# Optimization experiments

Hardware: AMD Instinct MI355X
Metric: run time of the kernel (lower is better)

Reference implementation:

```python
import jax, jax.numpy as jnp
import numpy as np
import math

N_HEAD = 12
BLOCK = 256  # local attention block size (ls)
EPS = 1e-6


def _rotate(x):
    # pairs (a, b) -> (-b, a) over last dim (matches rotate_embeddings)
    a = x[..., 0::2]
    b = x[..., 1::2]
    return jnp.stack([-b, a], axis=-1).reshape(x.shape)


def setup_inputs() -> dict:
    key = jax.random.key(0)
    k1, k2, k3 = jax.random.split(key, 3)
    B, T, C = 4, 8192, 768
    s = 0.02
    return {
        "x": jax.random.normal(k1, (B, T, C), jnp.float32),
        "w_qkv": jax.random.normal(k2, (C, 3 * C), jnp.float32) * s,
        "w_ln": jnp.ones((C,), jnp.float32),
        "w_proj": jax.random.normal(k3, (C, C), jnp.float32) * s,
    }


def reference(x, w_qkv, w_ln, w_proj):
    B, T, C = x.shape
    nh, ls = N_HEAD, BLOCK
    hd = C // nh
    ng = T // ls

    xb = x.reshape(B, ng, ls, C)
    qkv = xb @ w_qkv                                   # (B,ng,ls,3C)
    q, k, v = jnp.split(qkv, 3, axis=-1)

    # QK RMSNorm over full embedding dim (before head split)
    def rms(t):
        return t * jax.lax.rsqrt(jnp.mean(t * t, axis=-1, keepdims=True) + EPS) * w_ln
    q, k = rms(q), rms(k)

    # split heads: (B,ng,nh,ls,hd)
    def heads(t):
        return jnp.swapaxes(t.reshape(B, ng, ls, nh, hd), 2, 3)
    q, k, v = heads(q), heads(k), heads(v)

    # RoPE (repo layout: freqs tiled via cat((ts,ts)), interleaved pair rotation)
    pos = 10000.0 ** ((-2.0 * jnp.arange(0, hd, 2, dtype=jnp.float32) - 1.0) / hd)
    ts = jnp.arange(ls, dtype=jnp.float32)[:, None] * pos[None, :]   # (ls, hd/2)
    rot = jnp.concatenate([ts, ts], axis=-1)                          # (ls, hd)
    cos, sin = jnp.cos(rot), jnp.sin(rot)
    q = q * cos + _rotate(q) * sin
    k = k * cos + _rotate(k) * sin

    # block-causal scores: causal only within each local block
    scale = 1.0 / math.sqrt(hd)
    att = jnp.einsum('bgnqd,bgnkd->bgnqk', q, k) * scale              # (B,ng,nh,ls,ls)
    mask = jnp.tril(jnp.ones((ls, ls), dtype=bool))
    att = jnp.where(mask, att, -jnp.finfo(att.dtype).max)
    att = jax.nn.softmax(att, axis=-1)
    y = jnp.einsum('bgnqk,bgnkd->bgnqd', att, v)                      # (B,ng,nh,ls,hd)

    y = jnp.swapaxes(y, 2, 3).reshape(B, ng, ls, C)
    y = y @ w_proj
    return y.reshape(B, T, C)
```

## Files before the change

kernel.cpp:

```cpp
#include <hip/hip_runtime.h>
#include <math.h>

typedef __attribute__((ext_vector_type(8))) short bf16x8;
typedef __attribute__((ext_vector_type(4))) short bf16x4;
typedef __attribute__((ext_vector_type(2))) short bf16x2;
typedef __attribute__((ext_vector_type(4))) float f32x4;

#define NH 12
#define HD 64
#define C0 768
#define C3 2304
#define LS 256

static __device__ __forceinline__ float bf2f(short u) {
  union { unsigned int i; float f; } c;
  c.i = ((unsigned int)(unsigned short)u) << 16;
  return c.f;
}
static __device__ __forceinline__ short f2bf(float f) {
  union { float f; unsigned int i; } c; c.f = f;
  unsigned int x = c.i;
  x += 0x7fffu + ((x >> 16) & 1u);
  return (short)(x >> 16);
}
static __device__ __forceinline__ unsigned pk2(float a, float b) {
  return (unsigned)(unsigned short)f2bf(a) | ((unsigned)(unsigned short)f2bf(b) << 16);
}

static __device__ __forceinline__ void gload_lds16(const short* g, const short* l) {
  unsigned long long ga = (unsigned long long)g;
  unsigned int la = (unsigned int)(unsigned long long)l;
  __builtin_amdgcn_global_load_lds(
      (const __attribute__((address_space(1))) void*)ga,
      (__attribute__((address_space(3))) void*)la, 16, 0, 0);
}

__global__ __launch_bounds__(256) void cast_kernel(const float* __restrict__ in,
                                                   short* __restrict__ out, int nquads) {
  int i = blockIdx.x * blockDim.x + threadIdx.x;
  int stride = gridDim.x * blockDim.x;
  for (; i < nquads; i += stride) {
    float4 v = ((const float4*)in)[i];
    bf16x4 o = { f2bf(v.x), f2bf(v.y), f2bf(v.z), f2bf(v.w) };
    ((bf16x4*)out)[i] = o;
  }
}

__global__ __launch_bounds__(256) void cast_transpose_kernel(const float* __restrict__ in,
                                                             short* __restrict__ out,
                                                             int K, int N) {
  __shared__ float tile[32][33];
  int n0 = blockIdx.x * 32, k0 = blockIdx.y * 32;
  int tx = threadIdx.x & 31, ty = threadIdx.x >> 5;
#pragma unroll
  for (int i = 0; i < 32; i += 8)
    tile[ty + i][tx] = in[(long)(k0 + ty + i) * N + n0 + tx];
  __syncthreads();
#pragma unroll
  for (int i = 0; i < 32; i += 8)
    out[(long)(n0 + ty + i) * K + k0 + tx] = f2bf(tile[tx][ty + i]);
}

__global__ void rope_tab_kernel(float* __restrict__ cost, float* __restrict__ sint) {
  int t = blockIdx.x, d = threadIdx.x;
  int i = d & 31;
  float freq = powf(10000.0f, -(float)(4 * i + 1) / 64.0f);
  float th = (float)t * freq;
  cost[t * 64 + d] = cosf(th);
  sint[t * 64 + d] = sinf(th);
}

template <int OUT_F32>
__global__ __launch_bounds__(256) void gemm_kernel(const short* __restrict__ A,
                                                   const short* __restrict__ Bt,
                                                   void* __restrict__ Cout,
                                                   int N, int K) {
  __shared__ short As[128 * 64];
  __shared__ short Bs[128 * 64];
  int bn = blockIdx.x, bm = blockIdx.y;
  int t = threadIdx.x, lane = t & 63, wave = t >> 6;
  int lr = lane & 15, lg = lane >> 4;
  int wm = (wave >> 1) * 64, wn = (wave & 1) * 64;
  const short* Abase = A + (long)bm * 128 * K;
  const short* Bbase = Bt + (long)bn * 128 * K;

  f32x4 zero4 = {0.f, 0.f, 0.f, 0.f};
  f32x4 acc[4][4];
#pragma unroll
  for (int m = 0; m < 4; ++m)
#pragma unroll
    for (int n = 0; n < 4; ++n) acc[m][n] = zero4;

  int srow[4], scol[4];
#pragma unroll
  for (int i = 0; i < 4; ++i) {
    int q = i * 256 + t;
    int r = q >> 3, cp = q & 7;
    srow[i] = r;
    scol[i] = (cp ^ (r & 7)) * 8;
  }

  for (int kt = 0; kt < K / 64; ++kt) {
    int k0 = kt * 64;
#pragma unroll
    for (int i = 0; i < 4; ++i) {
      int q = i * 256 + t;
      gload_lds16(Abase + (long)srow[i] * K + k0 + scol[i], &As[q * 8]);
      gload_lds16(Bbase + (long)srow[i] * K + k0 + scol[i], &Bs[q * 8]);
    }
    asm volatile("s_waitcnt vmcnt(0)" ::: "memory");
    __syncthreads();

#pragma unroll
    for (int s = 0; s < 2; ++s) {
      bf16x8 af[4], bfv[4];
#pragma unroll
      for (int m = 0; m < 4; ++m) {
        int row = wm + m * 16 + lr;
        af[m] = *(bf16x8*)&As[row * 64 + (((s * 4 + lg) ^ (row & 7)) << 3)];
      }
#pragma unroll
      for (int n = 0; n < 4; ++n) {
        int row = wn + n * 16 + lr;
        bfv[n] = *(bf16x8*)&Bs[row * 64 + (((s * 4 + lg) ^ (row & 7)) << 3)];
      }
#pragma unroll
      for (int m = 0; m < 4; ++m)
#pragma unroll
        for (int n = 0; n < 4; ++n)
          acc[m][n] = __builtin_amdgcn_mfma_f32_16x16x32_bf16(af[m], bfv[n], acc[m][n], 0, 0, 0);
    }
    __syncthreads();
  }

  long crow0 = (long)bm * 128 + wm;
  long ccol0 = (long)bn * 128 + wn;
#pragma unroll
  for (int m = 0; m < 4; ++m)
#pragma unroll
    for (int n = 0; n < 4; ++n)
#pragma unroll
      for (int r = 0; r < 4; ++r) {
        long row = crow0 + m * 16 + lg * 4 + r;
        long col = ccol0 + n * 16 + lr;
        float v = acc[m][n][r];
        if (OUT_F32) ((float*)Cout)[row * N + col] = v;
        else ((short*)Cout)[row * N + col] = f2bf(v);
      }
}

__global__ __launch_bounds__(384) void norm_rope_kernel(short* __restrict__ QKV,
    const float* __restrict__ w_ln, const float* __restrict__ cost,
    const float* __restrict__ sint) {
  int row = blockIdx.x;
  int t = row & 255;
  int i = threadIdx.x;
  long base = (long)row * C3;
  bf16x2 q2 = *(bf16x2*)&QKV[base + 2 * i];
  bf16x2 k2 = *(bf16x2*)&QKV[base + C0 + 2 * i];
  float qa = bf2f(q2.x), qb = bf2f(q2.y);
  float ka = bf2f(k2.x), kb = bf2f(k2.y);
  float sq = qa * qa + qb * qb;
  float sk = ka * ka + kb * kb;
#pragma unroll
  for (int o = 32; o > 0; o >>= 1) {
    sq += __shfl_down(sq, o);
    sk += __shfl_down(sk, o);
  }
  __shared__ float red[2][6];
  int wv = i >> 6;
  if ((i & 63) == 0) { red[0][wv] = sq; red[1][wv] = sk; }
  __syncthreads();
  float s0 = 0.f, s1 = 0.f;
#pragma unroll
  for (int w = 0; w < 6; ++w) { s0 += red[0][w]; s1 += red[1][w]; }
  float rq = rsqrtf(s0 * (1.0f / 768.0f) + 1e-6f);
  float rk = rsqrtf(s1 * (1.0f / 768.0f) + 1e-6f);
  float wl0 = w_ln[2 * i], wl1 = w_ln[2 * i + 1];
  float qn0 = qa * rq * wl0, qn1 = qb * rq * wl1;
  float kn0 = ka * rk * wl0, kn1 = kb * rk * wl1;
  int d0 = (2 * i) & 63;
  float c0 = cost[t * 64 + d0], c1 = cost[t * 64 + d0 + 1];
  float s0r = sint[t * 64 + d0], s1r = sint[t * 64 + d0 + 1];
  bf16x2 qo, ko;
  qo.x = f2bf(qn0 * c0 - qn1 * s0r);
  qo.y = f2bf(qn1 * c1 + qn0 * s1r);
  ko.x = f2bf(kn0 * c0 - kn1 * s0r);
  ko.y = f2bf(kn1 * c1 + kn0 * s1r);
  *(bf16x2*)&QKV[base + 2 * i] = qo;
  *(bf16x2*)&QKV[base + C0 + 2 * i] = ko;
}

__global__ __launch_bounds__(512, 3) void attn_kernel(const short* __restrict__ QKV,
                                                      short* __restrict__ Y) {
  __shared__ short Ks[256 * 64];
  __shared__ short Vt[64 * 256];
  int blk = blockIdx.x;
  int bg = blk / NH, h = blk % NH;
  const long base = (long)bg * LS * C3 + h * HD;
  int tid = threadIdx.x, lane = tid & 63, wave = tid >> 6;
  int lr = lane & 15, lg = lane >> 4;

#pragma unroll
  for (int it = 0; it < 4; ++it) {
    int q = it * 512 + tid;
    int row = q >> 3, cp = q & 7;
    int gcp = cp ^ (row & 7);
    gload_lds16(QKV + base + (long)row * C3 + C0 + gcp * 8, &Ks[q * 8]);
  }
#pragma unroll
  for (int it = 0; it < 8; ++it) {
    int e = tid * 4 + it * 2048;
    int k = e >> 6, n = e & 63;
    bf16x4 v = *(const bf16x4*)&QKV[base + (long)k * C3 + 2 * C0 + n];
#pragma unroll
    for (int j = 0; j < 4; ++j) {
      int nn = n + j;
      Vt[nn * 256 + (((k >> 3) ^ (nn & 7)) << 3) + (k & 7)] = v[j];
    }
  }
  asm volatile("s_waitcnt vmcnt(0)" ::: "memory");
  __syncthreads();

  int addrA = (((lane >> 4) & 1) * 32 + lr) * 4;
  int addrB = addrA + 64;
  bool selhi = (lane & 32) != 0;

  for (int tt = 0; tt < 2; ++tt) {
    int tile = (tt == 0) ? wave : (15 - wave);
    int m0 = tile * 16;
    bf16x8 qf[2];
#pragma unroll
    for (int ks = 0; ks < 2; ++ks)
      qf[ks] = *(const bf16x8*)&QKV[base + (long)(m0 + lr) * C3 + ks * 32 + lg * 8];

    f32x4 zero4 = {0.f, 0.f, 0.f, 0.f};
    f32x4 accs[16];
#pragma unroll
    for (int n = 0; n < 16; ++n) accs[n] = zero4;

    __builtin_amdgcn_s_setprio(1);
#pragma unroll
    for (int n = 0; n < 16; ++n) {
      if (n <= tile) {
        int row = n * 16 + lr, sw = row & 7;
        bf16x8 k0 = *(bf16x8*)&Ks[row * 64 + ((lg ^ sw) << 3)];
        bf16x8 k1 = *(bf16x8*)&Ks[row * 64 + (((4 + lg) ^ sw) << 3)];
        accs[n] = __builtin_amdgcn_mfma_f32_16x16x32_bf16(k0, qf[0], accs[n], 0, 0, 0);
        accs[n] = __builtin_amdgcn_mfma_f32_16x16x32_bf16(k1, qf[1], accs[n], 0, 0, 0);
      }
    }
    __builtin_amdgcn_s_setprio(0);

    float mloc = -1e30f;
#pragma unroll
    for (int n = 0; n < 16; ++n) {
      if (n <= tile) {
#pragma unroll
        for (int r = 0; r < 4; ++r) {
          float v = accs[n][r];
          if (n == tile) v = (lg * 4 + r <= lr) ? v : -1e30f;
          accs[n][r] = v;
          mloc = fmaxf(mloc, v);
        }
      }
    }
    mloc = fmaxf(mloc, __shfl_xor(mloc, 16));
    mloc = fmaxf(mloc, __shfl_xor(mloc, 32));
    float s = 0.f;
#pragma unroll
    for (int n = 0; n < 16; ++n) {
      if (n <= tile) {
#pragma unroll
        for (int r = 0; r < 4; ++r) {
          float p = __expf((accs[n][r] - mloc) * 0.125f);
          accs[n][r] = p;
          s += p;
        }
      }
    }
    s += __shfl_xor(s, 16);
    s += __shfl_xor(s, 32);
    float rs = 1.0f / s;
    float rv[4];
#pragma unroll
    for (int r = 0; r < 4; ++r) {
      union { float f; int i; } c; c.f = rs;
      union { int i; float f; } o;
      o.i = __builtin_amdgcn_ds_bpermute((lg * 4 + r) * 4, c.i);
      rv[r] = o.f;
    }

    int ktmax = (m0 + 15) >> 5;
    f32x4 yacc[4];
#pragma unroll
    for (int n2 = 0; n2 < 4; ++n2) yacc[n2] = zero4;
#pragma unroll
    for (int kt = 0; kt < 8; ++kt) {
      if (kt <= ktmax) {
        int n0 = 2 * kt, n1 = 2 * kt + 1;
        unsigned a01_0 = pk2(accs[n0][0], accs[n0][1]);
        unsigned a23_0 = pk2(accs[n0][2], accs[n0][3]);
        unsigned a01_1 = (n1 <= tile) ? pk2(accs[n1][0], accs[n1][1]) : 0u;
        unsigned a23_1 = (n1 <= tile) ? pk2(accs[n1][2], accs[n1][3]) : 0u;
        union { unsigned u[4]; bf16x8 v; } af;
        unsigned g0a = (unsigned)__builtin_amdgcn_ds_bpermute(addrA, (int)a01_0);
        unsigned g0b = (unsigned)__builtin_amdgcn_ds_bpermute(addrA, (int)a01_1);
        unsigned g1a = (unsigned)__builtin_amdgcn_ds_bpermute(addrA, (int)a23_0);
        unsigned g1b = (unsigned)__builtin_amdgcn_ds_bpermute(addrA, (int)a23_1);
        unsigned g2a = (unsigned)__builtin_amdgcn_ds_bpermute(addrB, (int)a01_0);
        unsigned g2b = (unsigned)__builtin_amdgcn_ds_bpermute(addrB, (int)a01_1);
        unsigned g3a = (unsigned)__builtin_amdgcn_ds_bpermute(addrB, (int)a23_0);
        unsigned g3b = (unsigned)__builtin_amdgcn_ds_bpermute(addrB, (int)a23_1);
        af.u[0] = selhi ? g0b : g0a;
        af.u[1] = selhi ? g1b : g1a;
        af.u[2] = selhi ? g2b : g2a;
        af.u[3] = selhi ? g3b : g3a;
        int ac = kt * 32 + lg * 8;
        __builtin_amdgcn_s_setprio(1);
#pragma unroll
        for (int n2 = 0; n2 < 4; ++n2) {
          int vn = n2 * 16 + lr;
          bf16x8 vb = *(bf16x8*)&Vt[vn * 256 + (((ac >> 3) ^ (vn & 7)) << 3)];
          yacc[n2] = __builtin_amdgcn_mfma_f32_16x16x32_bf16(af.v, vb, yacc[n2], 0, 0, 0);
        }
        __builtin_amdgcn_s_setprio(0);
      }
    }

#pragma unroll
    for (int n2 = 0; n2 < 4; ++n2) {
#pragma unroll
      for (int r = 0; r < 4; ++r) {
        int row = m0 + lg * 4 + r, d = n2 * 16 + lr;
        Y[((long)(bg * LS + row)) * C0 + h * HD + d] = f2bf(yacc[n2][r] * rv[r]);
      }
    }
  }
}

extern "C" void kernel_launch(void* const* d_in, const int* in_sizes, int n_in,
                              void* d_out, int out_size, void* d_ws, size_t ws_size,
                              hipStream_t stream) {
  (void)in_sizes; (void)n_in; (void)out_size; (void)ws_size;
  const float* x = (const float*)d_in[0];
  const float* w_qkv = (const float*)d_in[1];
  const float* w_ln = (const float*)d_in[2];
  const float* w_proj = (const float*)d_in[3];
  float* out = (float*)d_out;

  char* ws = (char*)d_ws;
  short* Xb      = (short*)(ws + 0);
  short* QKV     = (short*)(ws + 50331648);
  short* Yb      = (short*)(ws + 201326592);
  short* WqkvT   = (short*)(ws + 251658240);
  short* WprojT  = (short*)(ws + 255197184);
  float* cost    = (float*)(ws + 256376832);
  float* sint    = (float*)(ws + 256442368);

  cast_kernel<<<2048, 256, 0, stream>>>(x, Xb, (4 * 8192 * C0) / 4);
  cast_transpose_kernel<<<dim3(C3 / 32, C0 / 32), 256, 0, stream>>>(w_qkv, WqkvT, C0, C3);
  cast_transpose_kernel<<<dim3(C0 / 32, C0 / 32), 256, 0, stream>>>(w_proj, WprojT, C0, C0);
  rope_tab_kernel<<<256, 64, 0, stream>>>(cost, sint);

  gemm_kernel<0><<<dim3(C3 / 128, 32768 / 128), 256, 0, stream>>>(Xb, WqkvT, QKV, C3, C0);
  norm_rope_kernel<<<32768, 384, 0, stream>>>(QKV, w_ln, cost, sint);
  attn_kernel<<<128 * NH, 512, 0, stream>>>(QKV, Yb);
  gemm_kernel<1><<<dim3(C0 / 128, 32768 / 128), 256, 0, stream>>>(Yb, WprojT, out, C0, C0);
}
```

Before: 352.6 us.

## Replace GEMM with 256x256-tile, 8-wave, double-buffered pipelined MFMA kernel

Replaces the 128x128 single-buffered GEMM with a 256x256 tile kernel using 8 waves, a double-buffered 128KB LDS, fine-grained staged global-to-LDS loads interleaved with MFMA phases, s_setprio scheduling, and an XCD-aware block remapping. It is meant to hide global load latency and improve data reuse for both the QKV and output projections. Risks include the large LDS footprint limiting occupancy, and correctness depends on the vmcnt bookkeeping. For the 768-wide projection, only 384 blocks are launched.

```diff
diff --git a/kernel.cpp b/kernel.cpp
--- a/kernel.cpp
+++ b/kernel.cpp
@@ -70,80 +70,123 @@
   sint[t * 64 + d] = sinf(th);
 }
 
+#define PH_PRE                                         \
+  __builtin_amdgcn_s_barrier();                        \
+  asm volatile("s_waitcnt lgkmcnt(0)" ::: "memory");   \
+  __builtin_amdgcn_sched_barrier(0);                   \
+  __builtin_amdgcn_s_setprio(1);
+#define PH_POST                                        \
+  __builtin_amdgcn_s_setprio(0);                       \
+  __builtin_amdgcn_s_barrier();
+#define PH_POSTV                                       \
+  __builtin_amdgcn_s_setprio(0);                       \
+  asm volatile("s_waitcnt vmcnt(4)" ::: "memory");     \
+  __builtin_amdgcn_s_barrier();
+#define MMQ(MH, NP, AF)                                                            \
+  { _Pragma("unroll") for (int f_ = 0; f_ < 4; ++f_)                               \
+      _Pragma("unroll") for (int n_ = 0; n_ < 2; ++n_)                             \
+        _Pragma("unroll") for (int k_ = 0; k_ < 2; ++k_)                           \
+          acc[(MH)*4 + f_][(NP)*2 + n_] = __builtin_amdgcn_mfma_f32_16x16x32_bf16( \
+              AF[f_*2 + k_], bfv[((NP)*2 + n_)*2 + k_],                            \
+              acc[(MH)*4 + f_][(NP)*2 + n_], 0, 0, 0); }
+
 template <int OUT_F32>
-__global__ __launch_bounds__(256) void gemm_kernel(const short* __restrict__ A,
-                                                   const short* __restrict__ Bt,
-                                                   void* __restrict__ Cout,
-                                                   int N, int K) {
-  __shared__ short As[128 * 64];
-  __shared__ short Bs[128 * 64];
-  int bn = blockIdx.x, bm = blockIdx.y;
+__global__ __launch_bounds__(512, 2) void gemm8p_kernel(const short* __restrict__ A,
+                                                        const short* __restrict__ Bt,
+                                                        void* __restrict__ Cout,
+                                                        int N, int K, int nbn) {
+  __shared__ short lds[65536];
   int t = threadIdx.x, lane = t & 63, wave = t >> 6;
   int lr = lane & 15, lg = lane >> 4;
-  int wm = (wave >> 1) * 64, wn = (wave & 1) * 64;
-  const short* Abase = A + (long)bm * 128 * K;
-  const short* Bbase = Bt + (long)bn * 128 * K;
-
-  f32x4 zero4 = {0.f, 0.f, 0.f, 0.f};
-  f32x4 acc[4][4];
-#pragma unroll
-  for (int m = 0; m < 4; ++m)
-#pragma unroll
-    for (int n = 0; n < 4; ++n) acc[m][n] = zero4;
-
-  int srow[4], scol[4];
-#pragma unroll
-  for (int i = 0; i < 4; ++i) {
-    int q = i * 256 + t;
-    int r = q >> 3, cp = q & 7;
-    srow[i] = r;
-    scol[i] = (cp ^ (r & 7)) * 8;
-  }
-
-  for (int kt = 0; kt < K / 64; ++kt) {
-    int k0 = kt * 64;
-#pragma unroll
-    for (int i = 0; i < 4; ++i) {
-      int q = i * 256 + t;
-      gload_lds16(Abase + (long)srow[i] * K + k0 + scol[i], &As[q * 8]);
-      gload_lds16(Bbase + (long)srow[i] * K + k0 + scol[i], &Bs[q * 8]);
-    }
-    asm volatile("s_waitcnt vmcnt(0)" ::: "memory");
-    __syncthreads();
-
-#pragma unroll
-    for (int s = 0; s < 2; ++s) {
-      bf16x8 af[4], bfv[4];
-#pragma unroll
-      for (int m = 0; m < 4; ++m) {
-        int row = wm + m * 16 + lr;
-        af[m] = *(bf16x8*)&As[row * 64 + (((s * 4 + lg) ^ (row & 7)) << 3)];
-      }
-#pragma unroll
-      for (int n = 0; n < 4; ++n) {
-        int row = wn + n * 16 + lr;
-        bfv[n] = *(bf16x8*)&Bs[row * 64 + (((s * 4 + lg) ^ (row & 7)) << 3)];
-      }
-#pragma unroll
-      for (int m = 0; m < 4; ++m)
-#pragma unroll
-        for (int n = 0; n < 4; ++n)
-          acc[m][n] = __builtin_amdgcn_mfma_f32_16x16x32_bf16(af[m], bfv[n], acc[m][n], 0, 0, 0);
-    }
-    __syncthreads();
-  }
-
-  long crow0 = (long)bm * 128 + wm;
-  long ccol0 = (long)bn * 128 + wn;
-#pragma unroll
-  for (int m = 0; m < 4; ++m)
+  int wm = (wave >> 2) * 128, wn = (wave & 3) * 64;
+  int id = blockIdx.x;
+  int cpx = gridDim.x >> 3;
+  int sw = (id & 7) * cpx + (id >> 3);
+  int bm = sw / nbn, bn = sw % nbn;
+  const short* Abase = A + (long)bm * 256 * K;
+  const short* Bbase = Bt + (long)bn * 256 * K;
+  int srow = t >> 3;
+  int scol = ((t & 7) ^ (srow & 7)) * 8;
+  int smax = K >> 4;
+
+  f32x4 acc[8][4];
+#pragma unroll
+  for (int m = 0; m < 8; ++m)
+#pragma unroll
+    for (int n = 0; n < 4; ++n) acc[m][n] = (f32x4){0.f, 0.f, 0.f, 0.f};
+
+  auto STAGE = [&](int s) {
+    if (s < smax) {
+      int T = s >> 2, q = s & 3;
+      const short* base = (q < 2) ? Abase : Bbase;
+      const short* g = base + (long)((q & 1) * 128 + srow) * K + T * 64 + scol;
+      int lb = (T & 1) * 32768 + (q >> 1) * 16384 + (q & 1) * 8192 + t * 8;
+      gload_lds16(g, &lds[lb]);
+      gload_lds16(g + (long)64 * K, &lds[lb + 4096]);
+    }
+  };
+  auto LDA = [&](bf16x8* d, int b, int mh) {
+#pragma unroll
+    for (int f = 0; f < 4; ++f) {
+      int R = wm + mh * 64 + f * 16 + lr;
+      int rb = b * 32768 + R * 64;
+      int s8 = R & 7;
+      d[f * 2 + 0] = *(bf16x8*)&lds[rb + ((lg ^ s8) << 3)];
+      d[f * 2 + 1] = *(bf16x8*)&lds[rb + (((4 + lg) ^ s8) << 3)];
+    }
+  };
+  auto LDBH = [&](bf16x8* d, int b, int nh) {
+#pragma unroll
+    for (int j = 0; j < 2; ++j) {
+      int R = wn + (nh * 2 + j) * 16 + lr;
+      int rb = b * 32768 + 16384 + R * 64;
+      int s8 = R & 7;
+      d[(nh * 2 + j) * 2 + 0] = *(bf16x8*)&lds[rb + ((lg ^ s8) << 3)];
+      d[(nh * 2 + j) * 2 + 1] = *(bf16x8*)&lds[rb + (((4 + lg) ^ s8) << 3)];
+    }
+  };
+
+  STAGE(0); STAGE(1); STAGE(2); STAGE(3); STAGE(4); STAGE(5);
+  asm volatile("s_waitcnt vmcnt(4)" ::: "memory");
+  __builtin_amdgcn_s_barrier();
+
+  int iters = K >> 7;
+  for (int i = 0; i < iters; ++i) {
+    int si = 8 * i + 6;
+    bf16x8 af0[8], af1[8], bfv[8];
+    LDA(af0, 0, 0); LDBH(bfv, 0, 0);
+    STAGE(si + 0);
+    PH_PRE; MMQ(0, 0, af0); PH_POST;
+    LDA(af1, 0, 1); LDBH(bfv, 0, 1);
+    STAGE(si + 1);
+    PH_PRE; MMQ(0, 1, af0); PH_POST;
+    STAGE(si + 2);
+    PH_PRE; MMQ(1, 0, af1); PH_POST;
+    STAGE(si + 3);
+    PH_PRE; MMQ(1, 1, af1); PH_POSTV;
+    LDA(af0, 1, 0); LDBH(bfv, 1, 0);
+    STAGE(si + 4);
+    PH_PRE; MMQ(0, 0, af0); PH_POST;
+    LDA(af1, 1, 1); LDBH(bfv, 1, 1);
+    STAGE(si + 5);
+    PH_PRE; MMQ(0, 1, af0); PH_POST;
+    STAGE(si + 6);
+    PH_PRE; MMQ(1, 0, af1); PH_POST;
+    STAGE(si + 7);
+    PH_PRE; MMQ(1, 1, af1); PH_POSTV;
+  }
+
+  long crow0 = (long)bm * 256 + wm;
+  long ccol0 = (long)bn * 256 + wn;
+#pragma unroll
+  for (int f = 0; f < 8; ++f)
 #pragma unroll
     for (int n = 0; n < 4; ++n)
 #pragma unroll
       for (int r = 0; r < 4; ++r) {
-        long row = crow0 + m * 16 + lg * 4 + r;
+        long row = crow0 + (f >> 2) * 64 + (f & 3) * 16 + lg * 4 + r;
         long col = ccol0 + n * 16 + lr;
-        float v = acc[m][n][r];
+        float v = acc[f][n][r];
         if (OUT_F32) ((float*)Cout)[row * N + col] = v;
         else ((short*)Cout)[row * N + col] = f2bf(v);
       }
@@ -363,8 +406,10 @@
   cast_transpose_kernel<<<dim3(C0 / 32, C0 / 32), 256, 0, stream>>>(w_proj, WprojT, C0, C0);
   rope_tab_kernel<<<256, 64, 0, stream>>>(cost, sint);
 
-  gemm_kernel<0><<<dim3(C3 / 128, 32768 / 128), 256, 0, stream>>>(Xb, WqkvT, QKV, C3, C0);
+  gemm8p_kernel<0><<<(C3 / 256) * (32768 / 256), 512, 0, stream>>>(Xb, WqkvT, QKV,
+                                                                   C3, C0, C3 / 256);
   norm_rope_kernel<<<32768, 384, 0, stream>>>(QKV, w_ln, cost, sint);
   attn_kernel<<<128 * NH, 512, 0, stream>>>(QKV, Yb);
-  gemm_kernel<1><<<dim3(C0 / 128, 32768 / 128), 256, 0, stream>>>(Yb, WprojT, out, C0, C0);
-}
+  gemm8p_kernel<1><<<(C0 / 256) * (32768 / 256), 512, 0, stream>>>(Yb, WprojT, out,
+                                                                   C0, C0, C0 / 256);
+}
```

Measured after the change: 464.4 us. 31.7% more time.
